# Kernel optimization log

Measured on AMD Instinct MI355X. Metric: run time of the kernel, lower is better.

The kernel has to match this reference:

```python
import jax, jax.numpy as jnp
import numpy as np

B, C, H, W = 8, 1, 384, 384
INF2 = float(H * H + W * W + 1)  # 'infinite' squared distance


def _edt_single(feat):
    # Exact Euclidean distance transform: distance from every pixel to the
    # nearest True pixel in `feat` [H, W]. Separable squared-distance min.
    j = jnp.arange(W)
    dj2 = ((j[:, None] - j[None, :]).astype(jnp.float32)) ** 2  # [W, W']
    # g2[i, j] = min_{j': feat[i, j']} (j - j')^2
    g2 = jnp.min(jnp.where(feat[:, None, :], dj2[None, :, :], INF2), axis=2)  # [H, W]
    i = jnp.arange(H)
    di2 = ((i[:, None] - i[None, :]).astype(jnp.float32)) ** 2  # [H, H']
    # d2[i, j] = min_{i'} g2[i', j] + (i - i')^2
    d2 = jnp.min(di2[:, :, None] + g2[None, :, :], axis=1)  # [H, W]
    return jnp.sqrt(jnp.minimum(d2, INF2))


def _distance_map(target):
    # Signed distance map: EDT(1-m) - EDT(m), normalized by global max-abs,
    # matching BoundaryLoss._compute_distance_map (scipy distance_transform_edt).
    m = target.reshape(-1, H, W)

    def per_img(mi):
        fg = mi > 0.5
        pos = _edt_single(fg)        # dist to nearest foreground (EDT of 1-m)
        neg = _edt_single(~fg)       # dist to nearest background (EDT of m)
        return pos - neg

    dist = jax.lax.map(per_img, m).reshape(target.shape)
    maxabs = jnp.max(jnp.abs(dist))
    return jnp.where(maxabs > 0, dist / maxabs, dist)


def _lovasz_flat(logits, labels):
    # Binary Lovasz hinge on flat vectors (one sample).
    signs = 2.0 * labels - 1.0
    errors = 1.0 - logits * signs
    order = jnp.argsort(-errors)          # descending sort, perm is constant w.r.t. grads
    errors_sorted = errors[order]
    gt_sorted = labels[order]
    gts = jnp.sum(gt_sorted)
    intersection = gts - jnp.cumsum(gt_sorted)
    union = gts + jnp.cumsum(1.0 - gt_sorted)
    jaccard = 1.0 - intersection / (union + 1e-7)
    grad = jnp.concatenate([jaccard[:1], jaccard[1:] - jaccard[:-1]])
    return jnp.dot(jax.nn.relu(errors_sorted), grad)


def _combined_loss(pred, target):
    # BCE with logits (stable): max(x,0) - x*z + log1p(exp(-|x|)), mean.
    bce = jnp.mean(jnp.maximum(pred, 0.0) - pred * target + jnp.log1p(jnp.exp(-jnp.abs(pred))))
    # Dice.
    p = jax.nn.sigmoid(pred)
    smooth = 1.0
    intersection = jnp.sum(p * target)
    union = jnp.sum(p) + jnp.sum(target)
    dice = 1.0 - (2.0 * intersection + smooth) / (union + smooth)
    # Boundary: mean(sigmoid(pred) * signed_dist_map(target)); dist map is constant.
    dist_map = jax.lax.stop_gradient(_distance_map(target))
    boundary = jnp.mean(p * dist_map)
    # Lovasz hinge, per-sample over flattened pixels, then mean over batch.
    lovasz = jnp.mean(jax.vmap(_lovasz_flat)(pred.reshape(B, -1), target.reshape(B, -1)))
    loss = 0.3 * bce + 0.3 * dice + 0.2 * boundary + 0.2 * lovasz
    return jnp.clip(loss, 0.0, 100.0)


def setup_inputs() -> dict:
    key = jax.random.key(0)
    k1, k2 = jax.random.split(key)
    pred = jax.random.normal(k1, (B, C, H, W), dtype=jnp.float32)
    target = (jax.random.uniform(k2, (B, C, H, W)) < 0.3).astype(jnp.float32)
    return {"pred": pred, "target": target}


def reference(pred, target):
    return _combined_loss(pred, target)
```

## Files before the change

### kernel.cpp

```cpp
#include <hip/hip_runtime.h>
#include <hip/hip_bf16.h>
#include <math.h>

#define PSZ   147456
#define NTOT  1179648
#define WW    384
#define HH    384
#define NIMG  8
#define NBINH 2048
#define INF2F 294913.0f
#define GV2   1152
#define EBLK  768

static __device__ __forceinline__ float errval(float x, float z) {
    float s = __fsub_rn(__fmul_rn(2.0f, z), 1.0f);
    return __fsub_rn(1.0f, __fmul_rn(x, s));
}
static __device__ __forceinline__ int binof(float e) {
    int b = (int)(__fmul_rn(e, 256.0f));
    return b > (NBINH - 1) ? (NBINH - 1) : b;
}
static __device__ __forceinline__ float d2f(int d) {
    return (float)(d * d);
}

struct DPair { int df, db; };
static __device__ __forceinline__ DPair ndist2(const unsigned long long* __restrict__ m, int p) {
    const int BIG = 1 << 20;
    int q = p >> 6, b = p & 63;
    int df = BIG, db = BIG;
    {
        unsigned long long w = m[q];
        unsigned long long tf = w >> b;
        unsigned long long tb = (~w) >> b;
        if (tf) df = __builtin_ctzll(tf);
        if (tb) db = __builtin_ctzll(tb);
        for (int u = q + 1; (df == BIG || db == BIG) && u < 6; ++u) {
            w = m[u];
            if (df == BIG && w)  df = u * 64 + __builtin_ctzll(w)  - p;
            if (db == BIG && ~w) db = u * 64 + __builtin_ctzll(~w) - p;
        }
    }
    {
        unsigned long long w = m[q];
        unsigned long long tf = w << (63 - b);
        unsigned long long tb = (~w) << (63 - b);
        int lf = BIG, lb = BIG;
        if (tf) lf = __builtin_clzll(tf);
        if (tb) lb = __builtin_clzll(tb);
        for (int u = q - 1; (lf == BIG || lb == BIG) && u >= 0; --u) {
            w = m[u];
            if (lf == BIG && w)  lf = p - (u * 64 + 63 - __builtin_clzll(w));
            if (lb == BIG && ~w) lb = p - (u * 64 + 63 - __builtin_clzll(~w));
        }
        if (lf < df) df = lf;
        if (lb < db) db = lb;
    }
    DPair r;
    r.df = (df > 600) ? 600 : df;
    r.db = (db > 600) ? 600 : db;
    return r;
}

__global__ __launch_bounds__(256) void k_edth(const float* __restrict__ tgt,
                                              const float* __restrict__ pred,
                                              unsigned int* __restrict__ g2,
                                              unsigned long long* __restrict__ hist) {
    __shared__ unsigned long long h[NBINH * 2];
    for (int q = threadIdx.x; q < NBINH * 2; q += 256) h[q] = 0ull;
    __syncthreads();
    int img = blockIdx.x & 7;
    int bb  = blockIdx.x >> 3;
    int row = img * HH + bb * 4 + (threadIdx.x >> 6);
    int l = threadIdx.x & 63;
    const float* tr = tgt  + (size_t)row * WW;
    const float* pr = pred + (size_t)row * WW;
    float zv[6], xv[6];
    unsigned long long mf[6];
#pragma unroll
    for (int c = 0; c < 6; ++c) { zv[c] = tr[c * 64 + l]; xv[c] = pr[c * 64 + l]; }
#pragma unroll
    for (int c = 0; c < 6; ++c) mf[c] = __ballot(zv[c] > 0.5f);
    size_t ob = (size_t)row * WW;
#pragma unroll
    for (int c = 0; c < 6; ++c) {
        int p = c * 64 + l;
        DPair d = ndist2(mf, p);
        g2[ob + p] = (unsigned int)d.df | ((unsigned int)d.db << 16);
        float e = errval(xv[c], zv[c]);
        if (e > 0.0f) {
            int lab = (zv[c] > 0.5f) ? 1 : 0;
            unsigned long long add = (1ull << 46) |
                (unsigned long long)__fmul_rn(e, 16777216.0f);
            atomicAdd(&h[(binof(e) << 1) + lab], add);
        }
    }
    __syncthreads();
    unsigned long long* gh = hist + ((size_t)img * NBINH << 1);
    for (int q = threadIdx.x; q < NBINH * 2; q += 256) {
        unsigned long long v = h[q];
        if (v) atomicAdd(&gh[q], v);
    }
}

__global__ __launch_bounds__(256) void k_fused(const float* __restrict__ pred,
                                               const float* __restrict__ tgt,
                                               const unsigned int* __restrict__ g2,
                                               float* __restrict__ pB, float* __restrict__ pP,
                                               float* __restrict__ pPT, float* __restrict__ pBnd,
                                               unsigned int* __restrict__ pPc,
                                               unsigned int* __restrict__ maxabsBits) {
    int t = threadIdx.x;
    int img = blockIdx.x & 7;
    int bb  = blockIdx.x >> 3;
    int v   = bb * 256 + t;
    int j   = v % WW;
    int i0  = (v / WW) * 4;
    const unsigned int* g2i = g2 + (size_t)img * PSZ;
    unsigned int w[24];
#pragma unroll
    for (int k = 0; k < 24; ++k) {
        int rr = i0 - 8 + k;
        rr = rr < 0 ? 0 : (rr > HH - 1 ? HH - 1 : rr);
        w[k] = g2i[rr * WW + j];
    }
    float aF[4], aB[4];
#pragma unroll
    for (int m = 0; m < 4; ++m) {
        float f = INF2F, g = INF2F;
#pragma unroll
        for (int k = m; k <= m + 16; ++k) {
            float r2 = d2f(k - 8 - m);
            f = fminf(f, r2 + d2f((int)(w[k] & 0xffffu)));
            g = fminf(g, r2 + d2f((int)(w[k] >> 16)));
        }
        aF[m] = f; aB[m] = g;
    }
#pragma unroll
    for (int m = 0; m < 4; ++m) {
        int i = i0 + m;
        for (int r = 9; r < HH; ++r) {
            float r2 = d2f(r);
            if (r2 >= fmaxf(aF[m], aB[m])) break;
            int up = i - r, dn = i + r;
            if (up >= 0) {
                unsigned int ww = g2i[up * WW + j];
                aF[m] = fminf(aF[m], r2 + d2f((int)(ww & 0xffffu)));
                aB[m] = fminf(aB[m], r2 + d2f((int)(ww >> 16)));
            }
            if (dn < HH) {
                unsigned int ww = g2i[dn * WW + j];
                aF[m] = fminf(aF[m], r2 + d2f((int)(ww & 0xffffu)));
                aB[m] = fminf(aB[m], r2 + d2f((int)(ww >> 16)));
            }
        }
    }
    float vals[6] = {0.f, 0.f, 0.f, 0.f, 0.f, 0.f};
#pragma unroll
    for (int m = 0; m < 4; ++m) {
        int n = img * PSZ + (i0 + m) * WW + j;
        float x = pred[n], z = tgt[n];
        bool lab = z > 0.5f;
        float dv = lab ? -sqrtf(fminf(aB[m], INF2F)) : sqrtf(fminf(aF[m], INF2F));
        float bce = fmaxf(x, 0.0f) - x * z + log1pf(expf(-fabsf(x)));
        float p = 1.0f / (1.0f + expf(-x));
        vals[0] += bce; vals[1] += p;
        vals[2] += lab ? p : 0.0f;
        vals[3] += p * dv;
        vals[4] += lab ? 1.0f : 0.0f;
        vals[5] = fmaxf(vals[5], fabsf(dv));
    }
#pragma unroll
    for (int k = 0; k < 5; ++k)
#pragma unroll
        for (int off = 32; off; off >>= 1) vals[k] += __shfl_xor(vals[k], off);
#pragma unroll
    for (int off = 32; off; off >>= 1) vals[5] = fmaxf(vals[5], __shfl_xor(vals[5], off));
    __shared__ float sw[4][6];
    int wv = t >> 6, lnn = t & 63;
    if (lnn == 0) {
#pragma unroll
        for (int k = 0; k < 6; ++k) sw[wv][k] = vals[k];
    }
    __syncthreads();
    if (t < 6) {
        int k = t;
        if (k == 5) {
            float a = fmaxf(fmaxf(sw[0][5], sw[1][5]), fmaxf(sw[2][5], sw[3][5]));
            atomicMax(maxabsBits, __float_as_uint(a));
        } else {
            float a = sw[0][k] + sw[1][k] + sw[2][k] + sw[3][k];
            if (k == 0) pB[blockIdx.x] = a;
            else if (k == 1) pP[blockIdx.x] = a;
            else if (k == 2) pPT[blockIdx.x] = a;
            else if (k == 3) pBnd[blockIdx.x] = a;
            else pPc[blockIdx.x] = (unsigned int)(a + 0.5f);
        }
    }
}

__global__ __launch_bounds__(256) void k_scanlov(const unsigned long long* __restrict__ hist,
                                                 const unsigned int* __restrict__ pPc,
                                                 const float* __restrict__ pB, const float* __restrict__ pP,
                                                 const float* __restrict__ pPT, const float* __restrict__ pBnd,
                                                 double* __restrict__ sums,
                                                 unsigned int* __restrict__ Pfin) {
    int b = blockIdx.x, t = threadIdx.x;
    __shared__ double dred[256];
    __shared__ unsigned int ured[256];
    double mv[4] = {0.0, 0.0, 0.0, 0.0};
    unsigned int mc = 0;
    if (t < 144) {
        int q = b + 8 * t;
        mv[0] = (double)pB[q]; mv[1] = (double)pP[q];
        mv[2] = (double)pPT[q]; mv[3] = (double)pBnd[q];
        mc = pPc[q];
    }
    ured[t] = mc; __syncthreads();
    for (int s = 128; s > 0; s >>= 1) { if (t < s) ured[t] += ured[t + s]; __syncthreads(); }
    unsigned int Pfull = ured[0];
    __syncthreads();
#pragma unroll
    for (int a = 0; a < 4; ++a) {
        dred[t] = mv[a]; __syncthreads();
        for (int s = 128; s > 0; s >>= 1) { if (t < s) dred[t] += dred[t + s]; __syncthreads(); }
        if (t == 0) sums[b * 5 + a] = dred[0];
        __syncthreads();
    }
    const unsigned long long* hc = hist + ((size_t)b * NBINH << 1);
    int m0 = t * 8;
    unsigned int ln = 0, lp = 0;
    unsigned int hcn[8], hcp[8];
    unsigned long long hsn[8], hsp[8];
#pragma unroll
    for (int k = 0; k < 8; ++k) {
        unsigned long long vn = hc[2 * (m0 + k)], vp = hc[2 * (m0 + k) + 1];
        hcn[k] = (unsigned int)(vn >> 46); hcp[k] = (unsigned int)(vp >> 46);
        hsn[k] = vn & ((1ull << 46) - 1);  hsp[k] = vp & ((1ull << 46) - 1);
        ln += hcn[k]; lp += hcp[k];
    }
    int lane = t & 63, wv = t >> 6;
    unsigned int sln = ln, slp = lp;
#pragma unroll
    for (int off = 1; off < 64; off <<= 1) {
        unsigned int an = __shfl_up(sln, off);
        unsigned int ap = __shfl_up(slp, off);
        if (lane >= off) { sln += an; slp += ap; }
    }
    __shared__ unsigned int wN[4], wP[4];
    if (lane == 63) { wN[wv] = sln; wP[wv] = slp; }
    __syncthreads();
    unsigned int baseN = 0, baseP = 0, totN = 0, totP = 0;
#pragma unroll
    for (int q = 0; q < 4; ++q) {
        if (q < wv) { baseN += wN[q]; baseP += wP[q]; }
        totN += wN[q]; totP += wP[q];
    }
    unsigned int runN = baseN + sln - ln;
    unsigned int runP = baseP + slp - lp;
    const double EPS = 1e-7;
    const double SCL = 1.0 / 16777216.0;
    double P = (double)Pfull;
    double l = 0.0;
#pragma unroll
    for (int k = 0; k < 8; ++k) {
        unsigned int hn = hcn[k], hp = hcp[k];
        if (hn | hp) {
            double negAbove = (double)(totN - runN - hn);
            double D0 = P + negAbove + EPS;
            if (hp) l += ((double)hsp[k] * SCL) / D0;
            if (hn) {
                double pAbove = (double)(totP - runP);
                double D1 = D0 + (double)hn;
                l += (P - pAbove) * ((double)hsn[k] * SCL) / (D0 * D1);
            }
            runN += hn; runP += hp;
        }
    }
    dred[t] = l; __syncthreads();
    for (int s = 128; s > 0; s >>= 1) { if (t < s) dred[t] += dred[t + s]; __syncthreads(); }
    if (t == 0) { sums[b * 5 + 4] = dred[0]; Pfin[b] = Pfull; }
}

__global__ __launch_bounds__(64) void k_final(const double* __restrict__ sums,
                                              const unsigned int* __restrict__ Pfin,
                                              const unsigned int* __restrict__ maxabsBits,
                                              float* __restrict__ out) {
    if (threadIdx.x == 0) {
        double sumBCE = 0, sumP = 0, sumPT = 0, sumBD = 0, sumLV = 0, tsum = 0;
        for (int b = 0; b < NIMG; ++b) {
            sumBCE += sums[b * 5 + 0];
            sumP   += sums[b * 5 + 1];
            sumPT  += sums[b * 5 + 2];
            sumBD  += sums[b * 5 + 3];
            sumLV  += sums[b * 5 + 4];
            tsum   += (double)Pfin[b];
        }
        double bce = sumBCE / (double)NTOT;
        double dice = 1.0 - (2.0 * sumPT + 1.0) / (sumP + tsum + 1.0);
        float ma = __uint_as_float(maxabsBits[0]);
        double bnd = sumBD / (double)NTOT;
        if (ma > 0.0f) bnd = bnd / (double)ma;
        double lov = sumLV / (double)NIMG;
        double loss = 0.3 * bce + 0.3 * dice + 0.2 * bnd + 0.2 * lov;
        if (loss < 0.0) loss = 0.0;
        if (loss > 100.0) loss = 100.0;
        out[0] = (float)loss;
    }
}

extern "C" void kernel_launch(void* const* d_in, const int* in_sizes, int n_in,
                              void* d_out, int out_size, void* d_ws, size_t ws_size,
                              hipStream_t stream) {
    const float* pred = (const float*)d_in[0];
    const float* tgt  = (const float*)d_in[1];
    char* ws = (char*)d_ws;

    size_t off = 0;
    unsigned long long* hist = (unsigned long long*)(ws + off); off += (size_t)NIMG * NBINH * 2 * 8;
    unsigned int* maxabsBits = (unsigned int*)(ws + off); off += 64;
    size_t zeroBytes = off;
    off = (off + 1023) & ~(size_t)1023;
    double* sums = (double*)(ws + off); off += NIMG * 5 * 8;
    unsigned int* Pfin = (unsigned int*)(ws + off); off += NIMG * 4;
    off = (off + 63) & ~(size_t)63;
    float* pB   = (float*)(ws + off); off += (size_t)GV2 * 4;
    float* pP   = (float*)(ws + off); off += (size_t)GV2 * 4;
    float* pPT  = (float*)(ws + off); off += (size_t)GV2 * 4;
    float* pBnd = (float*)(ws + off); off += (size_t)GV2 * 4;
    unsigned int* pPc = (unsigned int*)(ws + off); off += (size_t)GV2 * 4;
    off = (off + 1023) & ~(size_t)1023;
    unsigned int* g2 = (unsigned int*)(ws + off); off += (size_t)NIMG * PSZ * 4;
    (void)off; (void)ws_size; (void)in_sizes; (void)n_in; (void)out_size;

    hipMemsetAsync(d_ws, 0, zeroBytes, stream);
    k_edth<<<EBLK, 256, 0, stream>>>(tgt, pred, g2, hist);
    k_fused<<<GV2, 256, 0, stream>>>(pred, tgt, g2, pB, pP, pPT, pBnd, pPc, maxabsBits);
    k_scanlov<<<NIMG, 256, 0, stream>>>(hist, pPc, pB, pP, pPT, pBnd, sums, Pfin);
    k_final<<<1, 64, 0, stream>>>(sums, Pfin, maxabsBits, (float*)d_out);
}
```

Before: 60.64 us.

## Split Lovasz histogram into separate kernel with per-partition histograms, drop memset

Moves the Lovasz error histogram out of the EDT kernel into a dedicated kernel that builds per-image, per-partition shared-memory histograms and stores them without global atomics. The scan kernel then sums the eight partitions per bin. The workspace memset is removed by zeroing the max-abs word inside the EDT kernel. This trades global atomics and a memset for an extra launch, a second read of the inputs, only 64 large blocks for the histogram pass, and more reads in the single-block-per-image scan.

```diff
diff --git a/kernel.cpp b/kernel.cpp
--- a/kernel.cpp
+++ b/kernel.cpp
@@ -11,6 +11,7 @@
 #define INF2F 294913.0f
 #define GV2   1152
 #define EBLK  768
+#define HPART 8
 
 static __device__ __forceinline__ float errval(float x, float z) {
     float s = __fsub_rn(__fmul_rn(2.0f, z), 1.0f);
@@ -63,44 +64,51 @@
 }
 
 __global__ __launch_bounds__(256) void k_edth(const float* __restrict__ tgt,
-                                              const float* __restrict__ pred,
                                               unsigned int* __restrict__ g2,
-                                              unsigned long long* __restrict__ hist) {
-    __shared__ unsigned long long h[NBINH * 2];
-    for (int q = threadIdx.x; q < NBINH * 2; q += 256) h[q] = 0ull;
-    __syncthreads();
+                                              unsigned int* __restrict__ maxabsBits) {
+    if (blockIdx.x == 0 && threadIdx.x == 0) maxabsBits[0] = 0u;
     int img = blockIdx.x & 7;
     int bb  = blockIdx.x >> 3;
     int row = img * HH + bb * 4 + (threadIdx.x >> 6);
     int l = threadIdx.x & 63;
-    const float* tr = tgt  + (size_t)row * WW;
-    const float* pr = pred + (size_t)row * WW;
-    float zv[6], xv[6];
+    const float* tr = tgt + (size_t)row * WW;
     unsigned long long mf[6];
 #pragma unroll
-    for (int c = 0; c < 6; ++c) { zv[c] = tr[c * 64 + l]; xv[c] = pr[c * 64 + l]; }
-#pragma unroll
-    for (int c = 0; c < 6; ++c) mf[c] = __ballot(zv[c] > 0.5f);
+    for (int c = 0; c < 6; ++c)
+        mf[c] = __ballot(tr[c * 64 + l] > 0.5f);
     size_t ob = (size_t)row * WW;
 #pragma unroll
     for (int c = 0; c < 6; ++c) {
         int p = c * 64 + l;
         DPair d = ndist2(mf, p);
         g2[ob + p] = (unsigned int)d.df | ((unsigned int)d.db << 16);
-        float e = errval(xv[c], zv[c]);
+    }
+}
+
+__global__ __launch_bounds__(1024) void k_hist(const float* __restrict__ pred,
+                                               const float* __restrict__ tgt,
+                                               unsigned long long* __restrict__ histp) {
+    __shared__ unsigned long long h[NBINH * 2];
+    for (int q = threadIdx.x; q < NBINH * 2; q += 1024) h[q] = 0ull;
+    __syncthreads();
+    int img  = blockIdx.x & 7;
+    int part = blockIdx.x >> 3;
+    int base = img * PSZ + part * (PSZ / HPART);
+#pragma unroll
+    for (int it = 0; it < PSZ / HPART / 1024; ++it) {
+        int n = base + it * 1024 + threadIdx.x;
+        float x = pred[n], z = tgt[n];
+        float e = errval(x, z);
         if (e > 0.0f) {
-            int lab = (zv[c] > 0.5f) ? 1 : 0;
+            int lab = (z > 0.5f) ? 1 : 0;
             unsigned long long add = (1ull << 46) |
                 (unsigned long long)__fmul_rn(e, 16777216.0f);
             atomicAdd(&h[(binof(e) << 1) + lab], add);
         }
     }
     __syncthreads();
-    unsigned long long* gh = hist + ((size_t)img * NBINH << 1);
-    for (int q = threadIdx.x; q < NBINH * 2; q += 256) {
-        unsigned long long v = h[q];
-        if (v) atomicAdd(&gh[q], v);
-    }
+    unsigned long long* gh = histp + ((size_t)blockIdx.x << 12);
+    for (int q = threadIdx.x; q < NBINH * 2; q += 1024) gh[q] = h[q];
 }
 
 __global__ __launch_bounds__(256) void k_fused(const float* __restrict__ pred,
@@ -199,7 +207,7 @@
     }
 }
 
-__global__ __launch_bounds__(256) void k_scanlov(const unsigned long long* __restrict__ hist,
+__global__ __launch_bounds__(256) void k_scanlov(const unsigned long long* __restrict__ histp,
                                                  const unsigned int* __restrict__ pPc,
                                                  const float* __restrict__ pB, const float* __restrict__ pP,
                                                  const float* __restrict__ pPT, const float* __restrict__ pBnd,
@@ -227,14 +235,19 @@
         if (t == 0) sums[b * 5 + a] = dred[0];
         __syncthreads();
     }
-    const unsigned long long* hc = hist + ((size_t)b * NBINH << 1);
     int m0 = t * 8;
     unsigned int ln = 0, lp = 0;
     unsigned int hcn[8], hcp[8];
     unsigned long long hsn[8], hsp[8];
 #pragma unroll
     for (int k = 0; k < 8; ++k) {
-        unsigned long long vn = hc[2 * (m0 + k)], vp = hc[2 * (m0 + k) + 1];
+        unsigned long long vn = 0ull, vp = 0ull;
+#pragma unroll
+        for (int pp = 0; pp < HPART; ++pp) {
+            const unsigned long long* hc = histp + ((size_t)(pp * 8 + b) << 12);
+            vn += hc[2 * (m0 + k)];
+            vp += hc[2 * (m0 + k) + 1];
+        }
         hcn[k] = (unsigned int)(vn >> 46); hcp[k] = (unsigned int)(vp >> 46);
         hsn[k] = vn & ((1ull << 46) - 1);  hsp[k] = vp & ((1ull << 46) - 1);
         ln += hcn[k]; lp += hcp[k];
@@ -317,9 +330,9 @@
     char* ws = (char*)d_ws;
 
     size_t off = 0;
-    unsigned long long* hist = (unsigned long long*)(ws + off); off += (size_t)NIMG * NBINH * 2 * 8;
+    unsigned long long* histp = (unsigned long long*)(ws + off);
+    off += (size_t)NIMG * HPART * NBINH * 2 * 8;
     unsigned int* maxabsBits = (unsigned int*)(ws + off); off += 64;
-    size_t zeroBytes = off;
     off = (off + 1023) & ~(size_t)1023;
     double* sums = (double*)(ws + off); off += NIMG * 5 * 8;
     unsigned int* Pfin = (unsigned int*)(ws + off); off += NIMG * 4;
@@ -333,9 +346,9 @@
     unsigned int* g2 = (unsigned int*)(ws + off); off += (size_t)NIMG * PSZ * 4;
     (void)off; (void)ws_size; (void)in_sizes; (void)n_in; (void)out_size;
 
-    hipMemsetAsync(d_ws, 0, zeroBytes, stream);
-    k_edth<<<EBLK, 256, 0, stream>>>(tgt, pred, g2, hist);
+    k_edth<<<EBLK, 256, 0, stream>>>(tgt, g2, maxabsBits);
+    k_hist<<<NIMG * HPART, 1024, 0, stream>>>(pred, tgt, histp);
     k_fused<<<GV2, 256, 0, stream>>>(pred, tgt, g2, pB, pP, pPT, pBnd, pPc, maxabsBits);
-    k_scanlov<<<NIMG, 256, 0, stream>>>(hist, pPc, pB, pP, pPT, pBnd, sums, Pfin);
+    k_scanlov<<<NIMG, 256, 0, stream>>>(histp, pPc, pB, pP, pPT, pBnd, sums, Pfin);
     k_final<<<1, 64, 0, stream>>>(sums, Pfin, maxabsBits, (float*)d_out);
 }
```

Result: faster. 49.46 us (-18.4%).
